# Kernel optimization log

Measured on AMD Instinct MI355X. Metric: run time of the kernel, lower is better.

The kernel has to match this reference:

```python
import jax, jax.numpy as jnp
import numpy as np

G, B, C, H, W, D = 4, 1, 128, 32, 32, 32
STS = 4          # super_token_size (cubic)
N_ITER = 2
NUM_HEADS = 8
EPS = 1e-12


def _unfold3(x):
    """x: [..., H, W, D] -> [..., 27, H, W, D]; 3x3x3 neighborhood, zero pad."""
    *lead, h, w, d = x.shape
    xp = jnp.pad(x, [(0, 0)] * len(lead) + [(1, 1), (1, 1), (1, 1)])
    patches = [xp[..., i:i + h, j:j + w, l:l + d]
               for i in range(3) for j in range(3) for l in range(3)]
    return jnp.stack(patches, axis=-4)


def _fold3(x):
    """x: [..., 27, H, W, D] -> [..., H, W, D]; adjoint of _unfold3 (scatter-add)."""
    *lead, k27, h, w, d = x.shape
    out = jnp.zeros((*lead, h + 2, w + 2, d + 2), x.dtype)
    k = 0
    for i in range(3):
        for j in range(3):
            for l in range(3):
                out = out.at[..., i:i + h, j:j + w, l:l + d].add(x[..., k, :, :, :])
                k += 1
    return out[..., 1:h + 1, 1:w + 1, 1:d + 1]


def _attention_p(x, w_qkv, w_proj, b_proj):
    """Full self-attention over all voxels of x: [Bt, C, h, w, d]."""
    bt, c, hh, ww, dd = x.shape
    n = hh * ww * dd
    hd = c // NUM_HEADS
    xf = x.reshape(bt, c, n)
    qkv = jnp.einsum('oc,bcn->bon', w_qkv, xf)          # [Bt, 3C, N] (1x1 conv3d, no bias)
    q, k, v = jnp.split(qkv, 3, axis=1)
    q = q.reshape(bt * NUM_HEADS, hd, n) * (hd ** -0.5)
    k = k.reshape(bt * NUM_HEADS, hd, n)
    v = v.reshape(bt * NUM_HEADS, hd, n)
    attn = jax.nn.softmax(jnp.einsum('bcm,bcn->bmn', q, k), axis=-1)
    o = jnp.einsum('bmn,bcn->bcm', attn, v).reshape(bt, c, n)
    o = jnp.einsum('oc,bcn->bon', w_proj, o) + b_proj[None, :, None]
    return o.reshape(bt, c, hh, ww, dd)


def setup_inputs() -> dict:
    key = jax.random.key(0)
    k1, k2, k3, k4 = jax.random.split(key, 4)
    return {
        'x': jax.random.normal(k1, (G, B, C, H, W, D), jnp.float32),
        'w_qkv': jax.random.normal(k2, (3 * C, C), jnp.float32) * 0.02,
        'w_proj': jax.random.normal(k3, (C, C), jnp.float32) * 0.02,
        'b_proj': jax.random.normal(k4, (C,), jnp.float32) * 0.02,
    }


def reference(x, w_qkv, w_proj, b_proj):
    g, b, c, hH, wW, dD = x.shape
    bt = g * b
    xb = x.reshape(bt, c, hH, wW, dD)
    s = STS
    hh, ww, dd = hH // s, wW // s, dD // s
    m, p = hh * ww * dd, s ** 3
    scale = c ** -0.5

    blocks = xb.reshape(bt, c, hh, s, ww, s, dd, s)
    super_t = blocks.mean(axis=(3, 5, 7))                                   # [Bt,C,hh,ww,dd]
    pixel = blocks.transpose(0, 2, 4, 6, 3, 5, 7, 1).reshape(bt, m, p, c)    # [Bt,M,P,C]

    def _aff(st):
        su = _unfold3(st).reshape(bt, c, 27, m).transpose(0, 3, 1, 2)        # [Bt,M,C,27]
        return jax.nn.softmax(jnp.einsum('bmpc,bmck->bmpk', pixel, su) * scale, axis=-1)

    # iterative clustering (torch.no_grad in original)
    st = super_t
    aff = None
    asum = None
    for idx in range(N_ITER):
        aff = _aff(st)                                                       # [Bt,M,P,27]
        asum = _fold3(aff.sum(2).transpose(0, 2, 1).reshape(bt, 27, hh, ww, dd))[:, None]  # [Bt,1,hh,ww,dd]
        if idx < N_ITER - 1:
            stn = jnp.einsum('bmpc,bmpk->bmck', pixel, aff)                  # [Bt,M,C,27]
            stn = _fold3(stn.transpose(0, 2, 3, 1).reshape(bt, c, 27, hh, ww, dd))
            st = stn / (asum[:, 0][:, None] + EPS) if False else stn / (asum + EPS)
    aff = jax.lax.stop_gradient(aff)
    asum = jax.lax.stop_gradient(asum)

    st = jnp.einsum('bmpc,bmpk->bmck', pixel, aff)
    st = _fold3(st.transpose(0, 2, 3, 1).reshape(bt, c, 27, hh, ww, dd))
    st = st / (asum + EPS)                                                   # [Bt,C,hh,ww,dd]

    st = _attention_p(st, w_qkv, w_proj, b_proj)                             # refine

    su = _unfold3(st).reshape(bt, c, 27, m).transpose(0, 3, 1, 2)            # [Bt,M,C,27]
    pix = jnp.einsum('bmck,bmpk->bmcp', su, aff)                             # [Bt,M,C,P]
    out = pix.reshape(bt, hh, ww, dd, c, s, s, s).transpose(0, 4, 1, 5, 2, 6, 3, 7)
    out = out.reshape(bt, c, hH, wW, dD)
    return out.reshape(g, b, c, hH, wW, dD)
```

## Files before the change

kernel.cpp:

```cpp
#include <hip/hip_runtime.h>

#define BT 4
#define NC 128
#define MM 512
#define PP 64
#define K27 27
#define GSC 0.08838834764831845f
#define EPSF 1e-12f


__global__ __launch_bounds__(256) void k_pack(const float* __restrict__ x,
                                              float* __restrict__ px,
                                              float* __restrict__ st0) {
    __shared__ float sl[128 * 36];
    const int blk = blockIdx.x & 255;
    const int phase = blockIdx.x >> 8;
    const int b = blk >> 6, gh = (blk >> 3) & 7, gw = blk & 7;
    const int tid = threadIdx.x;
    const int cL = tid >> 1, half = tid & 1;
    const int cW = tid & 127, gdh = tid >> 7;
    float acc[4] = {0.f, 0.f, 0.f, 0.f};
    const size_t xbase = (size_t)b * NC * 32768 + (size_t)(gh * 4) * 1024 + (size_t)(gw * 4) * 32;

    for (int t = 0; t < 2; ++t) {
        const int ij = phase * 2 + t;
        const int i = ij >> 2, j = ij & 3;
        if (t) __syncthreads();
        const float* xp = x + xbase + (size_t)cL * 32768 + i * 1024 + j * 32 + half * 16;
#pragma unroll
        for (int q = 0; q < 4; ++q) {
            float4 v = *(const float4*)(xp + q * 4);
            *(float4*)&sl[cL * 36 + half * 16 + q * 4] = v;
        }
        __syncthreads();
#pragma unroll
        for (int gg = 0; gg < 4; ++gg) {
            const int gd = gdh * 4 + gg;
            float4 v = *(const float4*)&sl[cW * 36 + gd * 4];
            const int m = gh * 64 + gw * 8 + gd;
            float* pp = px + ((size_t)(b * MM + m) * PP + (i * 16 + j * 4)) * NC + cW;
            pp[0 * NC] = v.x;
            pp[1 * NC] = v.y;
            pp[2 * NC] = v.z;
            pp[3 * NC] = v.w;
            acc[gg] += v.x + v.y + v.z + v.w;
        }
    }
#pragma unroll
    for (int gg = 0; gg < 4; ++gg) {
        const int gd = gdh * 4 + gg;
        const int m = gh * 64 + gw * 8 + gd;
        atomicAdd(&st0[((size_t)b * MM + m) * NC + cW], acc[gg] * (1.f / 64.f));
    }
}

__global__ __launch_bounds__(256) void k_unpack(const float* __restrict__ pxo,
                                                float* __restrict__ out) {
    __shared__ float sl[128 * 36];
    const int blk = blockIdx.x & 255;
    const int phase = blockIdx.x >> 8;
    const int b = blk >> 6, gh = (blk >> 3) & 7, gw = blk & 7;
    const int tid = threadIdx.x;
    const int cL = tid >> 1, half = tid & 1;
    const int cW = tid & 127, gdh = tid >> 7;
    const size_t obase = (size_t)b * NC * 32768 + (size_t)(gh * 4) * 1024 + (size_t)(gw * 4) * 32;

    for (int t = 0; t < 2; ++t) {
        const int ij = phase * 2 + t;
        const int i = ij >> 2, j = ij & 3;
        if (t) __syncthreads();
#pragma unroll
        for (int gg = 0; gg < 4; ++gg) {
            const int gd = gdh * 4 + gg;
            const int m = gh * 64 + gw * 8 + gd;
            const float* pp = pxo + ((size_t)(b * MM + m) * PP + (i * 16 + j * 4)) * NC + cW;
            sl[cW * 36 + gd * 4 + 0] = pp[0 * NC];
            sl[cW * 36 + gd * 4 + 1] = pp[1 * NC];
            sl[cW * 36 + gd * 4 + 2] = pp[2 * NC];
            sl[cW * 36 + gd * 4 + 3] = pp[3 * NC];
        }
        __syncthreads();
        float* op = out + obase + (size_t)cL * 32768 + i * 1024 + j * 32 + half * 16;
#pragma unroll
        for (int q = 0; q < 4; ++q)
            *(float4*)(op + q * 4) = *(const float4*)&sl[cL * 36 + half * 16 + q * 4];
    }
}

template <int STORE_AFF>
__global__ __launch_bounds__(256) void k_iter(const float* __restrict__ px,
                                              const float* __restrict__ st,
                                              float* __restrict__ stn,
                                              float* __restrict__ affsum,
                                              float* __restrict__ affout) {
    __shared__ float pix[64 * 128];
    __shared__ float aff[64 * 28];
    const int tid = threadIdx.x;
    const int wg = blockIdx.x;
    const int b = wg >> 9;
    const int m = wg & (MM - 1);
    const int gh = m >> 6, gw = (m >> 3) & 7, gd = m & 7;

    const float* pxt = px + (size_t)wg * PP * NC;
    for (int t = tid; t < 2048; t += 256) {
        const int p = t >> 5, cb = t & 31;
        float4 v = *(const float4*)(pxt + t * 4);
        *(float4*)&pix[p * 128 + ((cb ^ (p & 7)) << 2)] = v;
    }

    const int kq = tid >> 6;
    const int kb = kq * 7;
    const int selfoff = (b * MM + m) * NC;
    int soff[7];
    int vmask = 0;
#pragma unroll
    for (int j = 0; j < 7; ++j) {
        const int k = kb + j;
        soff[j] = selfoff;
        if (k < K27) {
            const int i3 = k / 9, j3 = (k / 3) % 3, l3 = k % 3;
            const int mh = gh + i3 - 1, mw = gw + j3 - 1, md = gd + l3 - 1;
            if ((unsigned)mh < 8u && (unsigned)mw < 8u && (unsigned)md < 8u) {
                soff[j] = (b * MM + (mh * 64 + mw * 8 + md)) * NC;
                vmask |= (1 << j);
            }
        }
    }
    vmask = __builtin_amdgcn_readfirstlane(vmask);
    __syncthreads();

    {
        const int lane = tid & 63;
        const int pg = lane & 15, cseg = lane >> 4;
        float a00=0,a01=0,a02=0,a03=0,a04=0,a05=0,a06=0;
        float a10=0,a11=0,a12=0,a13=0,a14=0,a15=0,a16=0;
        float a20=0,a21=0,a22=0,a23=0,a24=0,a25=0,a26=0;
        float a30=0,a31=0,a32=0,a33=0,a34=0,a35=0,a36=0;
#pragma unroll 1
        for (int step = 0; step < 8; ++step) {
            const int cb = step * 4 + cseg;
            const int cb4 = cb * 4;
            const float4 sv0 = *(const float4*)(st + soff[0] + cb4);
            const float4 sv1 = *(const float4*)(st + soff[1] + cb4);
            const float4 sv2 = *(const float4*)(st + soff[2] + cb4);
            const float4 sv3 = *(const float4*)(st + soff[3] + cb4);
            const float4 sv4 = *(const float4*)(st + soff[4] + cb4);
            const float4 sv5 = *(const float4*)(st + soff[5] + cb4);
            const float4 sv6 = *(const float4*)(st + soff[6] + cb4);
            const float4 pv0 = *(const float4*)&pix[(pg +  0) * 128 + ((cb ^ ((pg +  0) & 7)) << 2)];
            const float4 pv1 = *(const float4*)&pix[(pg + 16) * 128 + ((cb ^ ((pg + 16) & 7)) << 2)];
            const float4 pv2 = *(const float4*)&pix[(pg + 32) * 128 + ((cb ^ ((pg + 32) & 7)) << 2)];
            const float4 pv3 = *(const float4*)&pix[(pg + 48) * 128 + ((cb ^ ((pg + 48) & 7)) << 2)];
#define DOT4(sv, A0, A1, A2, A3)                                          \
            A0 += pv0.x*sv.x + pv0.y*sv.y + pv0.z*sv.z + pv0.w*sv.w;      \
            A1 += pv1.x*sv.x + pv1.y*sv.y + pv1.z*sv.z + pv1.w*sv.w;      \
            A2 += pv2.x*sv.x + pv2.y*sv.y + pv2.z*sv.z + pv2.w*sv.w;      \
            A3 += pv3.x*sv.x + pv3.y*sv.y + pv3.z*sv.z + pv3.w*sv.w;
            DOT4(sv0, a00, a10, a20, a30)
            DOT4(sv1, a01, a11, a21, a31)
            DOT4(sv2, a02, a12, a22, a32)
            DOT4(sv3, a03, a13, a23, a33)
            DOT4(sv4, a04, a14, a24, a34)
            DOT4(sv5, a05, a15, a25, a35)
            DOT4(sv6, a06, a16, a26, a36)
#undef DOT4
        }
        if (!(vmask &  1)) { a00=0; a10=0; a20=0; a30=0; }
        if (!(vmask &  2)) { a01=0; a11=0; a21=0; a31=0; }
        if (!(vmask &  4)) { a02=0; a12=0; a22=0; a32=0; }
        if (!(vmask &  8)) { a03=0; a13=0; a23=0; a33=0; }
        if (!(vmask & 16)) { a04=0; a14=0; a24=0; a34=0; }
        if (!(vmask & 32)) { a05=0; a15=0; a25=0; a35=0; }
        if (!(vmask & 64)) { a06=0; a16=0; a26=0; a36=0; }
#define RED(v) v += __shfl_xor(v, 16); v += __shfl_xor(v, 32);
        RED(a00) RED(a01) RED(a02) RED(a03) RED(a04) RED(a05) RED(a06)
        RED(a10) RED(a11) RED(a12) RED(a13) RED(a14) RED(a15) RED(a16)
        RED(a20) RED(a21) RED(a22) RED(a23) RED(a24) RED(a25) RED(a26)
        RED(a30) RED(a31) RED(a32) RED(a33) RED(a34) RED(a35) RED(a36)
#undef RED
        if (cseg == 0) {
            float* r0 = &aff[(pg +  0) * 28 + kb];
            r0[0]=a00; r0[1]=a01; r0[2]=a02; r0[3]=a03; r0[4]=a04; r0[5]=a05; r0[6]=a06;
            float* r1 = &aff[(pg + 16) * 28 + kb];
            r1[0]=a10; r1[1]=a11; r1[2]=a12; r1[3]=a13; r1[4]=a14; r1[5]=a15; r1[6]=a16;
            float* r2 = &aff[(pg + 32) * 28 + kb];
            r2[0]=a20; r2[1]=a21; r2[2]=a22; r2[3]=a23; r2[4]=a24; r2[5]=a25; r2[6]=a26;
            float* r3 = &aff[(pg + 48) * 28 + kb];
            r3[0]=a30; r3[1]=a31; r3[2]=a32; r3[3]=a33; r3[4]=a34; r3[5]=a35; r3[6]=a36;
        }
    }
    __syncthreads();

    {
        const int p = tid >> 2, sub4 = tid & 3;
        const int k0 = sub4 * 7;
        float row[7];
        float mx = -1e30f;
#pragma unroll
        for (int t = 0; t < 7; ++t) {
            if (k0 + t < K27) {
                row[t] = aff[p * 28 + k0 + t] * GSC;
                mx = fmaxf(mx, row[t]);
            }
        }
        mx = fmaxf(mx, __shfl_xor(mx, 1));
        mx = fmaxf(mx, __shfl_xor(mx, 2));
        float s = 0.f;
#pragma unroll
        for (int t = 0; t < 7; ++t) {
            if (k0 + t < K27) {
                row[t] = __expf(row[t] - mx);
                s += row[t];
            }
        }
        s += __shfl_xor(s, 1);
        s += __shfl_xor(s, 2);
        const float inv = 1.f / s;
#pragma unroll
        for (int t = 0; t < 7; ++t)
            if (k0 + t < K27) aff[p * 28 + k0 + t] = row[t] * inv;
        if (sub4 == 3) aff[p * 28 + 27] = 0.f;
    }
    __syncthreads();

    if (tid < 216) {
        const int k = tid >> 3, seg = tid & 7;
        float s = 0.f;
#pragma unroll
        for (int pp = 0; pp < 8; ++pp) s += aff[(seg * 8 + pp) * 28 + k];
        s += __shfl_xor(s, 1);
        s += __shfl_xor(s, 2);
        s += __shfl_xor(s, 4);
        if (seg == 0) affsum[((size_t)b * K27 + k) * MM + m] = s;
    }
    if (STORE_AFF) {
        const size_t base = (size_t)(b * MM + m) * PP * K27;
        for (int t = tid; t < PP * K27; t += 256) {
            int p = t / K27, k = t - p * K27;
            affout[base + t] = aff[p * 28 + k];
        }
    }

    {
        const int kq2 = tid >> 5, cq = tid & 31;
        if (kq2 < 7) {
            float c00=0,c01=0,c02=0,c03=0;
            float c10=0,c11=0,c12=0,c13=0;
            float c20=0,c21=0,c22=0,c23=0;
            float c30=0,c31=0,c32=0,c33=0;
#pragma unroll 2
            for (int p = 0; p < 64; ++p) {
                float4 pv = *(const float4*)&pix[p * 128 + ((cq ^ (p & 7)) << 2)];
                float4 av = *(const float4*)&aff[p * 28 + kq2 * 4];
                c00 += av.x * pv.x; c01 += av.x * pv.y; c02 += av.x * pv.z; c03 += av.x * pv.w;
                c10 += av.y * pv.x; c11 += av.y * pv.y; c12 += av.y * pv.z; c13 += av.y * pv.w;
                c20 += av.z * pv.x; c21 += av.z * pv.y; c22 += av.z * pv.z; c23 += av.z * pv.w;
                c30 += av.w * pv.x; c31 += av.w * pv.y; c32 += av.w * pv.z; c33 += av.w * pv.w;
            }
            const int k0 = kq2 * 4;
#pragma unroll
            for (int q = 0; q < 4; ++q) {
                const int k = k0 + q;
                if (k < K27) {
                    const int i3 = k / 9, j3 = (k / 3) % 3, l3 = k % 3;
                    const int mh = gh + i3 - 1, mw = gw + j3 - 1, md = gd + l3 - 1;
                    if ((unsigned)mh < 8u && (unsigned)mw < 8u && (unsigned)md < 8u) {
                        float4 w4 = (q == 0) ? make_float4(c00, c01, c02, c03)
                                  : (q == 1) ? make_float4(c10, c11, c12, c13)
                                  : (q == 2) ? make_float4(c20, c21, c22, c23)
                                             : make_float4(c30, c31, c32, c33);
                        *(float4*)&stn[(((size_t)b * K27 + k) * MM + m) * NC + cq * 4] = w4;
                    }
                }
            }
        }
    }
}

__global__ __launch_bounds__(128) void k_fold(const float* __restrict__ stn,
                                              const float* __restrict__ affsum,
                                              float* __restrict__ stout) {
    const int wg = blockIdx.x;
    const int b = wg >> 9, g = wg & (MM - 1);
    const int gh = g >> 6, gw = (g >> 3) & 7, gd = g & 7;
    const int c = threadIdx.x;
    float num = 0.f, den = 0.f;
#pragma unroll
    for (int k = 0; k < K27; ++k) {
        int i = k / 9, j = (k / 3) % 3, l = k % 3;
        int mh = gh + 1 - i, mw = gw + 1 - j, md = gd + 1 - l;
        if ((unsigned)mh < 8u && (unsigned)mw < 8u && (unsigned)md < 8u) {
            int mm = mh * 64 + mw * 8 + md;
            num += stn[(((size_t)b * K27 + k) * MM + mm) * NC + c];
            den += affsum[((size_t)b * K27 + k) * MM + mm];
        }
    }
    stout[((size_t)b * MM + g) * NC + c] = num / (den + EPSF);
}

template <int COUT, int BIAS>
__global__ __launch_bounds__(256) void k_linear(const float* __restrict__ in,
                                                const float* __restrict__ w,
                                                const float* __restrict__ bias,
                                                float* __restrict__ out) {
    __shared__ float sl[8 * 128];
    const int tid = threadIdx.x;
    const int g0 = blockIdx.x * 8;
    {
        const int row = tid >> 5, c4 = (tid & 31) * 4;
        float4 v = *(const float4*)(in + (size_t)(g0 + row) * NC + c4);
        *(float4*)&sl[row * 128 + c4] = v;
    }
    __syncthreads();

    if (COUT == 384) {
#pragma unroll
        for (int pass = 0; pass < 2; ++pass) {
            const int o = tid + pass * 256;
            if (o < COUT) {
                const float* wr = w + (size_t)o * NC;
                float acc[8];
#pragma unroll
                for (int r = 0; r < 8; ++r) acc[r] = BIAS ? bias[o] : 0.f;
#pragma unroll 2
                for (int cs = 0; cs < 8; ++cs) {
                    const int c = cs * 16;
                    const float4 w0 = *(const float4*)(wr + c);
                    const float4 w1 = *(const float4*)(wr + c + 4);
                    const float4 w2 = *(const float4*)(wr + c + 8);
                    const float4 w3 = *(const float4*)(wr + c + 12);
#pragma unroll
                    for (int r = 0; r < 8; ++r) {
                        const float* xr = &sl[r * 128 + c];
                        const float4 x0 = *(const float4*)(xr);
                        const float4 x1 = *(const float4*)(xr + 4);
                        const float4 x2 = *(const float4*)(xr + 8);
                        const float4 x3 = *(const float4*)(xr + 12);
                        acc[r] += w0.x*x0.x + w0.y*x0.y + w0.z*x0.z + w0.w*x0.w
                                + w1.x*x1.x + w1.y*x1.y + w1.z*x1.z + w1.w*x1.w
                                + w2.x*x2.x + w2.y*x2.y + w2.z*x2.z + w2.w*x2.w
                                + w3.x*x3.x + w3.y*x3.y + w3.z*x3.z + w3.w*x3.w;
                    }
                }
#pragma unroll
                for (int r = 0; r < 8; ++r)
                    out[(size_t)(g0 + r) * COUT + o] = acc[r];
            }
        }
    } else {
        const int o = tid & 127;
        const int rb = (tid >> 7) * 4;
        const float* wr = w + (size_t)o * NC;
        float acc[4];
#pragma unroll
        for (int r = 0; r < 4; ++r) acc[r] = BIAS ? bias[o] : 0.f;
#pragma unroll 2
        for (int cs = 0; cs < 8; ++cs) {
            const int c = cs * 16;
            const float4 w0 = *(const float4*)(wr + c);
            const float4 w1 = *(const float4*)(wr + c + 4);
            const float4 w2 = *(const float4*)(wr + c + 8);
            const float4 w3 = *(const float4*)(wr + c + 12);
#pragma unroll
            for (int r = 0; r < 4; ++r) {
                const float* xr = &sl[(rb + r) * 128 + c];
                const float4 x0 = *(const float4*)(xr);
                const float4 x1 = *(const float4*)(xr + 4);
                const float4 x2 = *(const float4*)(xr + 8);
                const float4 x3 = *(const float4*)(xr + 12);
                acc[r] += w0.x*x0.x + w0.y*x0.y + w0.z*x0.z + w0.w*x0.w
                        + w1.x*x1.x + w1.y*x1.y + w1.z*x1.z + w1.w*x1.w
                        + w2.x*x2.x + w2.y*x2.y + w2.z*x2.z + w2.w*x2.w
                        + w3.x*x3.x + w3.y*x3.y + w3.z*x3.z + w3.w*x3.w;
            }
        }
#pragma unroll
        for (int r = 0; r < 4; ++r)
            out[(size_t)(g0 + rb + r) * COUT + o] = acc[r];
    }
}

__global__ __launch_bounds__(256) void k_attn(const float* __restrict__ qkv,
                                              float* __restrict__ obuf) {
    __shared__ float po[4][64][17];
    __shared__ float pl[4][64];
    const int b = blockIdx.x >> 6;
    const int h = (blockIdx.x >> 3) & 7;
    const int mt = blockIdx.x & 7;
    const int tid = threadIdx.x;
    const int nseg = tid >> 6, lane = tid & 63;
    const int m = mt * 64 + lane;

    float q[16];
    {
        const float* qp = qkv + (size_t)(b * MM + m) * 384 + h * 16;
#pragma unroll
        for (int cc = 0; cc < 16; cc += 4) {
            float4 t4 = *(const float4*)(qp + cc);
            q[cc + 0] = t4.x * 0.25f;
            q[cc + 1] = t4.y * 0.25f;
            q[cc + 2] = t4.z * 0.25f;
            q[cc + 3] = t4.w * 0.25f;
        }
    }
    float o[16];
#pragma unroll
    for (int i = 0; i < 16; ++i) o[i] = 0.f;
    float lsum = 0.f;
    const float* kb = qkv + (size_t)b * MM * 384 + 128 + h * 16;
    for (int n = nseg * 128; n < nseg * 128 + 128; ++n) {
        const float* kr = kb + (size_t)n * 384;
        float s = 0.f;
#pragma unroll
        for (int cc = 0; cc < 16; cc += 4) {
            float4 kv4 = *(const float4*)(kr + cc);
            s += q[cc] * kv4.x + q[cc + 1] * kv4.y + q[cc + 2] * kv4.z + q[cc + 3] * kv4.w;
        }
        float e = __expf(s);
        lsum += e;
        const float* vr = kr + 128;
#pragma unroll
        for (int cc = 0; cc < 16; cc += 4) {
            float4 vv = *(const float4*)(vr + cc);
            o[cc + 0] += e * vv.x;
            o[cc + 1] += e * vv.y;
            o[cc + 2] += e * vv.z;
            o[cc + 3] += e * vv.w;
        }
    }
#pragma unroll
    for (int cc = 0; cc < 16; ++cc) po[nseg][lane][cc] = o[cc];
    pl[nseg][lane] = lsum;
    __syncthreads();
    {
        const int ml = tid & 63, ccq = tid >> 6;
        float lt = pl[0][ml] + pl[1][ml] + pl[2][ml] + pl[3][ml];
        float inv = 1.f / lt;
        float* op = obuf + (size_t)(b * MM + mt * 64 + ml) * NC + h * 16 + ccq * 4;
        float4 w4;
        w4.x = (po[0][ml][ccq * 4 + 0] + po[1][ml][ccq * 4 + 0] + po[2][ml][ccq * 4 + 0] + po[3][ml][ccq * 4 + 0]) * inv;
        w4.y = (po[0][ml][ccq * 4 + 1] + po[1][ml][ccq * 4 + 1] + po[2][ml][ccq * 4 + 1] + po[3][ml][ccq * 4 + 1]) * inv;
        w4.z = (po[0][ml][ccq * 4 + 2] + po[1][ml][ccq * 4 + 2] + po[2][ml][ccq * 4 + 2] + po[3][ml][ccq * 4 + 2]) * inv;
        w4.w = (po[0][ml][ccq * 4 + 3] + po[1][ml][ccq * 4 + 3] + po[2][ml][ccq * 4 + 3] + po[3][ml][ccq * 4 + 3]) * inv;
        *(float4*)op = w4;
    }
}

__global__ __launch_bounds__(256) void k_final(const float* __restrict__ st3,
                                               const float* __restrict__ affin,
                                               float* __restrict__ pxo) {
    __shared__ float su[K27 * 132];
    __shared__ float aff[PP * 28];
    const int tid = threadIdx.x;
    const int wg = blockIdx.x;
    const int b = wg >> 9;
    const int m = wg & (MM - 1);
    const int gh = m >> 6, gw = (m >> 3) & 7, gd = m & 7;

    for (int t = tid; t < K27 * 128; t += 256) {
        int k = t >> 7, c = t & 127;
        int i = k / 9, j = (k / 3) % 3, l = k % 3;
        int mh = gh + i - 1, mw = gw + j - 1, md = gd + l - 1;
        float v = 0.f;
        if ((unsigned)mh < 8u && (unsigned)mw < 8u && (unsigned)md < 8u)
            v = st3[((size_t)b * MM + (mh * 64 + mw * 8 + md)) * NC + c];
        su[k * 132 + c] = v;
    }
    {
        const size_t base = (size_t)(b * MM + m) * PP * K27;
        for (int t = tid; t < PP * K27; t += 256) {
            int p = t / K27, k = t - p * K27;
            aff[p * 28 + k] = affin[base + t];
        }
    }
    __syncthreads();

    const int cg = tid & 31;
    const int pg = tid >> 5;
    float acc[4][8];
#pragma unroll
    for (int q = 0; q < 4; ++q)
#pragma unroll
        for (int pp = 0; pp < 8; ++pp) acc[q][pp] = 0.f;
    for (int k = 0; k < K27; ++k) {
        float4 sv = *(const float4*)&su[k * 132 + cg * 4];
#pragma unroll
        for (int pp = 0; pp < 8; ++pp) {
            float av = aff[(pg * 8 + pp) * 28 + k];
            acc[0][pp] += sv.x * av;
            acc[1][pp] += sv.y * av;
            acc[2][pp] += sv.z * av;
            acc[3][pp] += sv.w * av;
        }
    }
    float* pb = pxo + (size_t)wg * PP * NC;
#pragma unroll
    for (int pp = 0; pp < 8; ++pp) {
        float4 w4;
        w4.x = acc[0][pp];
        w4.y = acc[1][pp];
        w4.z = acc[2][pp];
        w4.w = acc[3][pp];
        *(float4*)&pb[(pg * 8 + pp) * NC + cg * 4] = w4;
    }
}

extern "C" void kernel_launch(void* const* d_in, const int* in_sizes, int n_in,
                              void* d_out, int out_size, void* d_ws, size_t ws_size,
                              hipStream_t stream) {
    (void)in_sizes; (void)n_in; (void)out_size; (void)ws_size;
    const float* x = (const float*)d_in[0];
    const float* w_qkv = (const float*)d_in[1];
    const float* w_proj = (const float*)d_in[2];
    const float* b_proj = (const float*)d_in[3];
    float* out = (float*)d_out;

    float* ws = (float*)d_ws;
    float* px = ws;
    float* st0 = px + (size_t)BT * MM * PP * NC;
    float* st1 = st0 + (size_t)BT * MM * NC;
    float* st2 = st1 + (size_t)BT * MM * NC;
    float* st3 = st2 + (size_t)BT * MM * NC;
    float* qkvb = st3 + (size_t)BT * MM * NC;
    float* obuf = qkvb + (size_t)BT * MM * 384;
    float* stn = obuf + (size_t)BT * MM * NC;
    float* afs = stn + (size_t)BT * K27 * MM * NC;
    float* aff1 = afs + (size_t)BT * K27 * MM;

    hipMemsetAsync(st0, 0, (size_t)BT * MM * NC * sizeof(float), stream);
    hipLaunchKernelGGL(k_pack, dim3(2048), dim3(256), 0, stream, x, px, st0);
    hipLaunchKernelGGL((k_iter<0>), dim3(BT * MM), dim3(256), 0, stream, px, st0, stn, afs, aff1);
    hipLaunchKernelGGL(k_fold, dim3(BT * MM), dim3(128), 0, stream, stn, afs, st1);
    hipLaunchKernelGGL((k_iter<1>), dim3(BT * MM), dim3(256), 0, stream, px, st1, stn, afs, aff1);
    hipLaunchKernelGGL(k_fold, dim3(BT * MM), dim3(128), 0, stream, stn, afs, st2);
    hipLaunchKernelGGL((k_linear<384, 0>), dim3(BT * MM / 8), dim3(256), 0, stream, st2, w_qkv, b_proj, qkvb);
    hipLaunchKernelGGL(k_attn, dim3(256), dim3(256), 0, stream, qkvb, obuf);
    hipLaunchKernelGGL((k_linear<128, 1>), dim3(BT * MM / 8), dim3(256), 0, stream, obuf, w_proj, b_proj, st3);
    hipLaunchKernelGGL(k_final, dim3(BT * MM), dim3(256), 0, stream, st3, aff1, px);
    hipLaunchKernelGGL(k_unpack, dim3(2048), dim3(256), 0, stream, px, out);
}
```

Baseline: 375.8 us.

## Fuse fold into iteration kernel via atomic scatter-add and deferred normalization

Removes the separate k_fold kernels and the large per-neighbor stn buffer (BT*27*MM*NC floats). Each iteration block now scatter-adds its numerator contributions and affinity sums straight into per-supertoken num/den buffers with atomics. The division by the denominator is deferred into the consumer (the next k_iter and the qkv linear). This saves two launches and a large write/read round-trip, at the cost of many scalar float atomics with contention and nondeterministic summation order.

```diff
diff --git a/kernel.cpp b/kernel.cpp
--- a/kernel.cpp
+++ b/kernel.cpp
@@ -87,11 +87,12 @@
     }
 }
 
-template <int STORE_AFF>
+template <int STORE_AFF, int DIV>
 __global__ __launch_bounds__(256) void k_iter(const float* __restrict__ px,
                                               const float* __restrict__ st,
-                                              float* __restrict__ stn,
-                                              float* __restrict__ affsum,
+                                              const float* __restrict__ den_in,
+                                              float* __restrict__ num_out,
+                                              float* __restrict__ den_out,
                                               float* __restrict__ affout) {
     __shared__ float pix[64 * 128];
     __shared__ float aff[64 * 28];
@@ -127,6 +128,12 @@
         }
     }
     vmask = __builtin_amdgcn_readfirstlane(vmask);
+    float inv[7];
+    if (DIV) {
+#pragma unroll
+        for (int j = 0; j < 7; ++j)
+            inv[j] = 1.f / (den_in[soff[j] >> 7] + EPSF);
+    }
     __syncthreads();
 
     {
@@ -165,6 +172,15 @@
             DOT4(sv6, a06, a16, a26, a36)
 #undef DOT4
         }
+        if (DIV) {
+            a00*=inv[0]; a10*=inv[0]; a20*=inv[0]; a30*=inv[0];
+            a01*=inv[1]; a11*=inv[1]; a21*=inv[1]; a31*=inv[1];
+            a02*=inv[2]; a12*=inv[2]; a22*=inv[2]; a32*=inv[2];
+            a03*=inv[3]; a13*=inv[3]; a23*=inv[3]; a33*=inv[3];
+            a04*=inv[4]; a14*=inv[4]; a24*=inv[4]; a34*=inv[4];
+            a05*=inv[5]; a15*=inv[5]; a25*=inv[5]; a35*=inv[5];
+            a06*=inv[6]; a16*=inv[6]; a26*=inv[6]; a36*=inv[6];
+        }
         if (!(vmask &  1)) { a00=0; a10=0; a20=0; a30=0; }
         if (!(vmask &  2)) { a01=0; a11=0; a21=0; a31=0; }
         if (!(vmask &  4)) { a02=0; a12=0; a22=0; a32=0; }
@@ -215,10 +231,10 @@
         }
         s += __shfl_xor(s, 1);
         s += __shfl_xor(s, 2);
-        const float inv = 1.f / s;
+        const float inv2 = 1.f / s;
 #pragma unroll
         for (int t = 0; t < 7; ++t)
-            if (k0 + t < K27) aff[p * 28 + k0 + t] = row[t] * inv;
+            if (k0 + t < K27) aff[p * 28 + k0 + t] = row[t] * inv2;
         if (sub4 == 3) aff[p * 28 + 27] = 0.f;
     }
     __syncthreads();
@@ -231,7 +247,12 @@
         s += __shfl_xor(s, 1);
         s += __shfl_xor(s, 2);
         s += __shfl_xor(s, 4);
-        if (seg == 0) affsum[((size_t)b * K27 + k) * MM + m] = s;
+        if (seg == 0) {
+            const int i3 = k / 9, j3 = (k / 3) % 3, l3 = k % 3;
+            const int mh = gh + i3 - 1, mw = gw + j3 - 1, md = gd + l3 - 1;
+            if ((unsigned)mh < 8u && (unsigned)mw < 8u && (unsigned)md < 8u)
+                atomicAdd(&den_out[b * MM + (mh * 64 + mw * 8 + md)], s);
+        }
     }
     if (STORE_AFF) {
         const size_t base = (size_t)(b * MM + m) * PP * K27;
@@ -269,7 +290,11 @@
                                   : (q == 1) ? make_float4(c10, c11, c12, c13)
                                   : (q == 2) ? make_float4(c20, c21, c22, c23)
                                              : make_float4(c30, c31, c32, c33);
-                        *(float4*)&stn[(((size_t)b * K27 + k) * MM + m) * NC + cq * 4] = w4;
+                        float* dst = &num_out[(size_t)(b * MM + (mh * 64 + mw * 8 + md)) * NC + cq * 4];
+                        atomicAdd(dst + 0, w4.x);
+                        atomicAdd(dst + 1, w4.y);
+                        atomicAdd(dst + 2, w4.z);
+                        atomicAdd(dst + 3, w4.w);
                     }
                 }
             }
@@ -277,29 +302,9 @@
     }
 }
 
-__global__ __launch_bounds__(128) void k_fold(const float* __restrict__ stn,
-                                              const float* __restrict__ affsum,
-                                              float* __restrict__ stout) {
-    const int wg = blockIdx.x;
-    const int b = wg >> 9, g = wg & (MM - 1);
-    const int gh = g >> 6, gw = (g >> 3) & 7, gd = g & 7;
-    const int c = threadIdx.x;
-    float num = 0.f, den = 0.f;
-#pragma unroll
-    for (int k = 0; k < K27; ++k) {
-        int i = k / 9, j = (k / 3) % 3, l = k % 3;
-        int mh = gh + 1 - i, mw = gw + 1 - j, md = gd + 1 - l;
-        if ((unsigned)mh < 8u && (unsigned)mw < 8u && (unsigned)md < 8u) {
-            int mm = mh * 64 + mw * 8 + md;
-            num += stn[(((size_t)b * K27 + k) * MM + mm) * NC + c];
-            den += affsum[((size_t)b * K27 + k) * MM + mm];
-        }
-    }
-    stout[((size_t)b * MM + g) * NC + c] = num / (den + EPSF);
-}
-
-template <int COUT, int BIAS>
+template <int COUT, int BIAS, int DIVIN>
 __global__ __launch_bounds__(256) void k_linear(const float* __restrict__ in,
+                                                const float* __restrict__ den,
                                                 const float* __restrict__ w,
                                                 const float* __restrict__ bias,
                                                 float* __restrict__ out) {
@@ -309,6 +314,10 @@
     {
         const int row = tid >> 5, c4 = (tid & 31) * 4;
         float4 v = *(const float4*)(in + (size_t)(g0 + row) * NC + c4);
+        if (DIVIN) {
+            const float dinv = 1.f / (den[g0 + row] + EPSF);
+            v.x *= dinv; v.y *= dinv; v.z *= dinv; v.w *= dinv;
+        }
         *(float4*)&sl[row * 128 + c4] = v;
     }
     __syncthreads();
@@ -518,24 +527,22 @@
     float* ws = (float*)d_ws;
     float* px = ws;
     float* st0 = px + (size_t)BT * MM * PP * NC;
-    float* st1 = st0 + (size_t)BT * MM * NC;
-    float* st2 = st1 + (size_t)BT * MM * NC;
-    float* st3 = st2 + (size_t)BT * MM * NC;
+    float* numA = st0 + (size_t)BT * MM * NC;
+    float* denA = numA + (size_t)BT * MM * NC;
+    float* numB = denA + (size_t)BT * MM;
+    float* denB = numB + (size_t)BT * MM * NC;
+    float* st3 = denB + (size_t)BT * MM;
     float* qkvb = st3 + (size_t)BT * MM * NC;
     float* obuf = qkvb + (size_t)BT * MM * 384;
-    float* stn = obuf + (size_t)BT * MM * NC;
-    float* afs = stn + (size_t)BT * K27 * MM * NC;
-    float* aff1 = afs + (size_t)BT * K27 * MM;
-
-    hipMemsetAsync(st0, 0, (size_t)BT * MM * NC * sizeof(float), stream);
+    float* aff1 = obuf + (size_t)BT * MM * NC;
+
+    hipMemsetAsync(st0, 0, ((size_t)BT * MM * NC * 3 + (size_t)BT * MM * 2) * sizeof(float), stream);
     hipLaunchKernelGGL(k_pack, dim3(2048), dim3(256), 0, stream, x, px, st0);
-    hipLaunchKernelGGL((k_iter<0>), dim3(BT * MM), dim3(256), 0, stream, px, st0, stn, afs, aff1);
-    hipLaunchKernelGGL(k_fold, dim3(BT * MM), dim3(128), 0, stream, stn, afs, st1);
-    hipLaunchKernelGGL((k_iter<1>), dim3(BT * MM), dim3(256), 0, stream, px, st1, stn, afs, aff1);
-    hipLaunchKernelGGL(k_fold, dim3(BT * MM), dim3(128), 0, stream, stn, afs, st2);
-    hipLaunchKernelGGL((k_linear<384, 0>), dim3(BT * MM / 8), dim3(256), 0, stream, st2, w_qkv, b_proj, qkvb);
+    hipLaunchKernelGGL((k_iter<0, 0>), dim3(BT * MM), dim3(256), 0, stream, px, st0, (const float*)nullptr, numA, denA, (float*)nullptr);
+    hipLaunchKernelGGL((k_iter<1, 1>), dim3(BT * MM), dim3(256), 0, stream, px, numA, denA, numB, denB, aff1);
+    hipLaunchKernelGGL((k_linear<384, 0, 1>), dim3(BT * MM / 8), dim3(256), 0, stream, numB, denB, w_qkv, b_proj, qkvb);
     hipLaunchKernelGGL(k_attn, dim3(256), dim3(256), 0, stream, qkvb, obuf);
-    hipLaunchKernelGGL((k_linear<128, 1>), dim3(BT * MM / 8), dim3(256), 0, stream, obuf, w_proj, b_proj, st3);
+    hipLaunchKernelGGL((k_linear<128, 1, 0>), dim3(BT * MM / 8), dim3(256), 0, stream, obuf, (const float*)nullptr, w_proj, b_proj, st3);
     hipLaunchKernelGGL(k_final, dim3(BT * MM), dim3(256), 0, stream, st3, aff1, px);
     hipLaunchKernelGGL(k_unpack, dim3(2048), dim3(256), 0, stream, px, out);
 }
```

Result: slower. 482.3 us (+28.4%).
